# Optimization experiments

Measured on AMD Instinct MI355X. Metric: run time of the kernel, lower is better.

## Reference

```python
import jax, jax.numpy as jnp
import numpy as np

B, N, H, W = 4, 16, 480, 640
Hf, Wf, C = 120, 160, 128
NUM_CLASSES = 14
NUM_EXPERTS = NUM_CLASSES - 1  # 13 per-class ROI experts
ROI = 14  # ROI-align output resolution


def setup_inputs() -> dict:
    key = jax.random.key(0)
    ks = jax.random.split(key, 20)
    inp = {
        'depth': jax.random.normal(ks[0], (B, 1, H, W), jnp.float32),
        'context': jax.random.normal(ks[1], (B, 192, Hf, Wf), jnp.float32),
        'input_feature_map': jax.random.normal(ks[2], (B, C, Hf, Wf), jnp.float32),
        'bin_num': 64,
        'min_depth': 1,
        'max_depth': 10,
        'masks': jax.random.uniform(ks[3], (B, N, Hf, Wf), jnp.float32),
        'instances': jax.random.uniform(ks[4], (B, N, H, W), jnp.float32),
        'boxes': jax.random.uniform(ks[5], (B, N, 4), jnp.float32),
        'labels': jax.random.randint(ks[6], (B, N), 0, NUM_EXPERTS),
    }
    s = 0.05
    # per-class (expert) parameters, stacked on leading expert axis
    inp['w_conv_s'] = s * jax.random.normal(ks[7], (NUM_EXPERTS, C, C, 3, 3), jnp.float32)
    inp['b_conv_s'] = jnp.zeros((NUM_EXPERTS, C), jnp.float32)
    inp['w_fc'] = s * jax.random.normal(ks[8], (NUM_EXPERTS, 2, C), jnp.float32)
    inp['b_fc'] = jnp.zeros((NUM_EXPERTS, 2), jnp.float32)
    inp['w_conv_c1'] = s * jax.random.normal(ks[9], (NUM_EXPERTS, 64, C, 3, 3), jnp.float32)
    inp['b_conv_c1'] = jnp.zeros((NUM_EXPERTS, 64), jnp.float32)
    inp['w_conv_c2'] = s * jax.random.normal(ks[10], (NUM_EXPERTS, 1, 64, 3, 3), jnp.float32)
    inp['b_conv_c2'] = jnp.zeros((NUM_EXPERTS, 1), jnp.float32)
    return inp


def _boxes_norm(boxes_flat):
    # map raw rand [M,4] -> valid normalized (y1,x1,y2,x2) in [0,1]
    y1 = 0.6 * boxes_flat[:, 0]
    x1 = 0.6 * boxes_flat[:, 1]
    y2 = y1 + 0.1 + 0.3 * boxes_flat[:, 2]
    x2 = x1 + 0.1 + 0.3 * boxes_flat[:, 3]
    return y1, x1, y2, x2


def _roi_align(fmap, batch_idx, boxes_flat, R):
    # fmap [B,C,Hf,Wf] -> [M,C,R,R] bilinear ROI sampling (irregular gather)
    _, _, hf, wf = fmap.shape
    y1, x1, y2, x2 = _boxes_norm(boxes_flat)
    t = (jnp.arange(R, dtype=fmap.dtype) + 0.5) / R
    ys = (y1[:, None] + (y2 - y1)[:, None] * t) * (hf - 1)  # [M,R]
    xs = (x1[:, None] + (x2 - x1)[:, None] * t) * (wf - 1)
    y0 = jnp.clip(jnp.floor(ys).astype(jnp.int32), 0, hf - 2)
    x0 = jnp.clip(jnp.floor(xs).astype(jnp.int32), 0, wf - 2)
    wy = jnp.clip(ys - y0, 0.0, 1.0)[:, :, None, None]   # [M,R,1,1]
    wx = jnp.clip(xs - x0, 0.0, 1.0)[:, None, :, None]   # [M,1,R,1]
    b = batch_idx[:, None, None]
    Y0 = y0[:, :, None]
    X0 = x0[:, None, :]
    def g(dy, dx):
        return fmap[b, :, Y0 + dy, X0 + dx]  # [M,R,R,C]
    out = (g(0, 0) * (1 - wy) * (1 - wx) + g(0, 1) * (1 - wy) * wx
           + g(1, 0) * wy * (1 - wx) + g(1, 1) * wy * wx)
    return jnp.transpose(out, (0, 3, 1, 2))  # [M,C,R,R]


def _conv(x, w, b):
    # x [Cin,R,R], w [Cout,Cin,3,3] -> [Cout,R,R]
    y = jax.lax.conv_general_dilated(x[None], w, (1, 1), 'SAME',
                                     dimension_numbers=('NCHW', 'OIHW', 'NCHW'))[0]
    return y + b[:, None, None]

_conv_v = jax.vmap(_conv)  # per-instance expert conv (per-instance weights)


def reference(depth, context, input_feature_map, bin_num, min_depth, max_depth,
              masks, instances, boxes, labels,
              w_conv_s, b_conv_s, w_fc, b_fc, w_conv_c1, b_conv_c1, w_conv_c2, b_conv_c2):
    b_, n_, h, w = instances.shape
    M = b_ * n_
    lab = labels.reshape(M)
    batch_idx = jnp.repeat(jnp.arange(b_), n_)
    boxes_flat = boxes.reshape(M, 4)

    # shared ROI gather of class-routed instances
    roi = _roi_align(input_feature_map, batch_idx, boxes_flat, ROI)  # [M,C,R,R]

    # hard routing: gather each instance's class-expert weights by label
    hs = jax.nn.relu(_conv_v(roi, w_conv_s[lab], b_conv_s[lab]))     # [M,C,R,R]
    gap = hs.mean(axis=(2, 3))                                        # [M,C]
    ss = jnp.einsum('mc,moc->mo', gap, w_fc[lab]) + b_fc[lab]         # [M,2]
    scale = ss[:, 0].reshape(b_, n_)
    shift = ss[:, 1].reshape(b_, n_)

    h1 = jax.nn.relu(_conv_v(roi, w_conv_c1[lab], b_conv_c1[lab]))    # [M,64,R,R]
    c = _conv_v(h1, w_conv_c2[lab], b_conv_c2[lab])                   # [M,1,R,R]
    canonical = jax.image.resize(c, (M, 1, h, w), method='bilinear')
    canonical = canonical.reshape(b_, n_, h, w)

    # loss_type == 0: relu(.).clamp(min=0.001) == max(., 0.001)
    depth_r = jnp.maximum(canonical * scale[..., None, None] + shift[..., None, None], 0.001)
    return depth_r, canonical, scale, shift
```

## Files before the change

### kernel.cpp

```cpp
#include <hip/hip_runtime.h>


typedef unsigned short bfu;
typedef __attribute__((ext_vector_type(8))) short bf16x8;
typedef __attribute__((ext_vector_type(4))) float f32x4;

__device__ __forceinline__ float bf2f(bfu u) {
  union { unsigned int i; float f; } v;
  v.i = ((unsigned int)u) << 16;
  return v.f;
}
__device__ __forceinline__ bfu f2bf(float f) {
  union { float f; unsigned int i; } v;
  v.f = f;
  unsigned int u = v.i;
  u = (u + 0x7fffu + ((u >> 16) & 1u)) >> 16;
  return (bfu)u;
}

#define B_  4
#define N_  16
#define M_  64
#define H_  480
#define W_  640
#define HF  120
#define WF  160
#define C_  128
#define R_  14
#define PIX 196
#define NE  13
#define KK  1152

#define WS_XB    0
#define WS_XH    802816
#define WS_C     1204224
#define WS_GAP   1216768
#define WS_SCALE 1224960
#define WS_SHIFT 1225024
#define WS_WF    1225088
#define WS_BIASF 2662784
#define WS_W2    2665280
#define WS_B2    2672768
#define WS_WFC   2672784
#define WS_BFC   2676112

__global__ __launch_bounds__(256) void prep_kernel(
    const float* __restrict__ w_s, const float* __restrict__ b_s,
    const float* __restrict__ w_fc, const float* __restrict__ b_fc,
    const float* __restrict__ w_c1, const float* __restrict__ b_c1,
    const float* __restrict__ w_c2, const float* __restrict__ b_c2,
    float* __restrict__ ws)
{
  const int P0 = NE*192*KK;
  const int P1 = NE*192;
  const int P2 = NE*576;
  const int P3 = NE;
  const int P4 = NE*256;
  const int P5 = NE*2;
  const int P6 = M_*C_;
  int total = P0+P1+P2+P3+P4+P5+P6;
  bfu* wf = (bfu*)(ws + WS_WF);
  for (int idx = blockIdx.x*256 + threadIdx.x; idx < total; idx += gridDim.x*256) {
    int d = idx;
    if (d < P0) {
      int e = d / (192*KK);
      int r = d - e*(192*KK);
      int oc = r / KK;
      int k  = r - oc*KK;
      int kidx = k >> 7, ic = k & 127;
      float v = (oc < 128) ? w_s[((e*128 + oc)*128 + ic)*9 + kidx]
                           : w_c1[((e*64 + (oc-128))*128 + ic)*9 + kidx];
      wf[d] = f2bf(v);
      continue;
    }
    d -= P0;
    if (d < P1) {
      int e = d / 192, oc = d - e*192;
      ws[WS_BIASF + d] = (oc < 128) ? b_s[e*128 + oc] : b_c1[e*64 + oc - 128];
      continue;
    }
    d -= P1;
    if (d < P2) {
      int e = d / 576, k = d - e*576;
      int kidx = k >> 6, ic = k & 63;
      ws[WS_W2 + d] = w_c2[(e*64 + ic)*9 + kidx];
      continue;
    }
    d -= P2;
    if (d < P3) { ws[WS_B2 + d] = b_c2[d]; continue; }
    d -= P3;
    if (d < P4) { ws[WS_WFC + d] = w_fc[d]; continue; }
    d -= P4;
    if (d < P5) { ws[WS_BFC + d] = b_fc[d]; continue; }
    d -= P5;
    ws[WS_GAP + d] = 0.f;
  }
}

__global__ __launch_bounds__(256) void xb_kernel(
    const float* __restrict__ fmap, const float* __restrict__ boxes,
    float* __restrict__ ws)
{
  __shared__ int iy0[R_], ix0[R_];
  __shared__ float swy[R_], swx[R_];
  int m = blockIdx.x;
  int tid = threadIdx.x;
  if (tid < 2*R_) {
    int r = tid % R_;
    bool isY = tid < R_;
    float b0 = boxes[m*4 + (isY ? 0 : 1)];
    float b2 = boxes[m*4 + (isY ? 2 : 3)];
    float lo = 0.6f * b0;
    float hi = lo + 0.1f + 0.3f * b2;
    float t = ((float)r + 0.5f) / (float)R_;
    float dim = isY ? (float)(HF-1) : (float)(WF-1);
    float s = (lo + (hi - lo) * t) * dim;
    int maxi = isY ? (HF-2) : (WF-2);
    int i0 = (int)floorf(s);
    i0 = i0 < 0 ? 0 : (i0 > maxi ? maxi : i0);
    float w = s - (float)i0;
    w = w < 0.f ? 0.f : (w > 1.f ? 1.f : w);
    if (isY) { iy0[r] = i0; swy[r] = w; } else { ix0[r] = i0; swx[r] = w; }
  }
  __syncthreads();
  int bi = m / N_;
  const float* fb = fmap + (size_t)bi * C_ * HF * WF;
  bfu* xb = (bfu*)(ws + WS_XB);
  for (int idx = tid; idx < PIX*64; idx += 256) {
    int ic2 = (idx & 63) * 2;
    int p = idx >> 6;
    int ry = p / R_, rx = p - (p/R_)*R_;
    int y0 = iy0[ry], x0 = ix0[rx];
    float wy = swy[ry], wx = swx[rx];
    float w00 = (1.f-wy)*(1.f-wx), w01 = (1.f-wy)*wx;
    float w10 = wy*(1.f-wx),       w11 = wy*wx;
    bfu pk[2];
    #pragma unroll
    for (int u = 0; u < 2; ++u) {
      const float* f = fb + ((size_t)(ic2+u)*HF + y0)*WF + x0;
      float v = f[0]*w00 + f[1]*w01 + f[WF]*w10 + f[WF+1]*w11;
      pk[u] = f2bf(v);
    }
    *(ushort2*)&xb[((size_t)m*PIX + p)*128 + ic2] = make_ushort2(pk[0], pk[1]);
  }
}

__global__ __launch_bounds__(256) void gemm_kernel(
    const int* __restrict__ labels, float* __restrict__ ws)
{
  __shared__ bfu lA[128*32];
  __shared__ bfu lB[128*32];
  const bfu* Xb = (const bfu*)(ws + WS_XB);
  const bfu* WFp = (const bfu*)(ws + WS_WF);
  const float* biasf = ws + WS_BIASF;
  float* gap = ws + WS_GAP;
  bfu* Xh = (bfu*)(ws + WS_XH);

  int bx = blockIdx.x;
  int m  = bx >> 2;
  int mb = (bx >> 1) & 1;
  int nb = bx & 1;
  int e = labels[m];
  int tid = threadIdx.x;
  int wave = tid >> 6, lane = tid & 63;
  int wm = wave >> 1, wn = wave & 1;
  int l15 = lane & 15, q = lane >> 4;

  int row0 = tid >> 2, row1 = row0 + 64;
  int kc = tid & 3;
  int loff0 = row0*32 + (kc ^ ((row0 >> 1) & 3))*8;
  int loff1 = row1*32 + (kc ^ ((row1 >> 1) & 3))*8;
  int g0 = mb*128 + row0, g1 = mb*128 + row1;
  bool av0 = g0 < 192, av1 = g1 < 192;
  const bfu* wfe = WFp + (size_t)e*192*KK;
  const bfu* wr0 = wfe + (size_t)g0*KK + kc*8;
  const bfu* wr1 = wfe + (size_t)g1*KK + kc*8;
  int pg0 = nb*128 + row0, pg1 = nb*128 + row1;
  int py0 = pg0 / 14, px0 = pg0 - (pg0/14)*14;
  int py1 = pg1 / 14, px1 = pg1 - (pg1/14)*14;
  bool pv0 = pg0 < PIX, pv1 = pg1 < PIX;
  const bfu* xbm = Xb + (size_t)m*PIX*128;

  f32x4 acc[4][4];
  #pragma unroll
  for (int i = 0; i < 4; ++i)
    #pragma unroll
    for (int j = 0; j < 4; ++j)
      acc[i][j] = (f32x4){0.f, 0.f, 0.f, 0.f};

  const uint4 z4 = make_uint4(0,0,0,0);
  for (int s = 0; s < 36; ++s) {
    int kidx = s >> 2, icc = s & 3;
    int dy = kidx/3 - 1, dx = (kidx - (kidx/3)*3) - 1;
    uint4 a0 = av0 ? *(const uint4*)(wr0 + s*32) : z4;
    uint4 a1 = av1 ? *(const uint4*)(wr1 + s*32) : z4;
    int ys0 = py0 + dy, xs0 = px0 + dx;
    int ys1 = py1 + dy, xs1 = px1 + dx;
    bool v0 = pv0 && (unsigned)ys0 < 14u && (unsigned)xs0 < 14u;
    bool v1 = pv1 && (unsigned)ys1 < 14u && (unsigned)xs1 < 14u;
    uint4 b0 = v0 ? *(const uint4*)(xbm + (size_t)(ys0*14+xs0)*128 + icc*32 + kc*8) : z4;
    uint4 b1 = v1 ? *(const uint4*)(xbm + (size_t)(ys1*14+xs1)*128 + icc*32 + kc*8) : z4;
    __syncthreads();
    *(uint4*)&lA[loff0] = a0;
    *(uint4*)&lA[loff1] = a1;
    *(uint4*)&lB[loff0] = b0;
    *(uint4*)&lB[loff1] = b1;
    __syncthreads();
    bf16x8 af[4], bfr[4];
    #pragma unroll
    for (int i = 0; i < 4; ++i) {
      int r = wm*64 + i*16 + l15;
      af[i] = *(const bf16x8*)&lA[r*32 + (q ^ ((r >> 1) & 3))*8];
    }
    #pragma unroll
    for (int j = 0; j < 4; ++j) {
      int r = wn*64 + j*16 + l15;
      bfr[j] = *(const bf16x8*)&lB[r*32 + (q ^ ((r >> 1) & 3))*8];
    }
    #pragma unroll
    for (int i = 0; i < 4; ++i)
      #pragma unroll
      for (int j = 0; j < 4; ++j)
        acc[i][j] = __builtin_amdgcn_mfma_f32_16x16x32_bf16(af[i], bfr[j], acc[i][j], 0, 0, 0);
  }

  if (mb == 0) {
    #pragma unroll
    for (int i = 0; i < 4; ++i) {
      int ocb = wm*64 + i*16 + q*4;
      f32x4 bv = *(const f32x4*)&biasf[e*192 + ocb];
      #pragma unroll
      for (int r = 0; r < 4; ++r) {
        float sum = 0.f;
        #pragma unroll
        for (int j = 0; j < 4; ++j) {
          int p = nb*128 + wn*64 + j*16 + l15;
          float v = acc[i][j][r] + bv[r];
          v = v > 0.f ? v : 0.f;
          if (p < PIX) sum += v;
        }
        sum += __shfl_xor(sum, 1);
        sum += __shfl_xor(sum, 2);
        sum += __shfl_xor(sum, 4);
        sum += __shfl_xor(sum, 8);
        if (l15 == 0) atomicAdd(&gap[m*C_ + ocb + r], sum);
      }
    }
  } else if (wm == 0) {
    #pragma unroll
    for (int i = 0; i < 4; ++i) {
      int icb = i*16 + q*4;
      f32x4 bv = *(const f32x4*)&biasf[e*192 + 128 + icb];
      #pragma unroll
      for (int j = 0; j < 4; ++j) {
        int p = nb*128 + wn*64 + j*16 + l15;
        if (p < PIX) {
          ushort4 pk;
          float v0 = acc[i][j][0] + bv[0]; v0 = v0 > 0.f ? v0 : 0.f;
          float v1 = acc[i][j][1] + bv[1]; v1 = v1 > 0.f ? v1 : 0.f;
          float v2 = acc[i][j][2] + bv[2]; v2 = v2 > 0.f ? v2 : 0.f;
          float v3 = acc[i][j][3] + bv[3]; v3 = v3 > 0.f ? v3 : 0.f;
          pk.x = f2bf(v0); pk.y = f2bf(v1); pk.z = f2bf(v2); pk.w = f2bf(v3);
          *(ushort4*)&Xh[((size_t)m*PIX + p)*64 + icb] = pk;
        }
      }
    }
  }
}

__global__ __launch_bounds__(128) void fc_kernel(
    const int* __restrict__ labels, float* __restrict__ ws,
    float* __restrict__ out)
{
  int t = threadIdx.x;
  int m = t >> 1, o = t & 1;
  int e = labels[m];
  const float* g = ws + WS_GAP + m*C_;
  const float* wv = ws + WS_WFC + (e*2 + o)*C_;
  float s = 0.f;
  for (int c = 0; c < C_; ++c) s += g[c] * wv[c];
  s = ws[WS_BFC + e*2 + o] + s * (1.f/(float)PIX);
  size_t base = (size_t)2 * M_ * H_ * W_;
  if (o == 0) { ws[WS_SCALE + m] = s; out[base + m] = s; }
  else        { ws[WS_SHIFT + m] = s; out[base + M_ + m] = s; }
}

__global__ __launch_bounds__(256) void convc2_kernel(
    const int* __restrict__ labels, float* __restrict__ ws)
{
  __shared__ bfu xh[PIX*64];
  __shared__ float w2l[576];
  int m = blockIdx.x;
  int e = labels[m];
  int tid = threadIdx.x;
  const bfu* Xh = (const bfu*)(ws + WS_XH) + (size_t)m*PIX*64;
  for (int i = tid; i < PIX*64/8; i += 256)
    *(uint4*)&xh[i*8] = *(const uint4*)&Xh[i*8];
  for (int i = tid; i < 576; i += 256)
    w2l[i] = ws[WS_W2 + e*576 + i];
  __syncthreads();
  if (tid < PIX) {
    int y = tid / 14, x = tid - (tid/14)*14;
    float acc = 0.f;
    #pragma unroll
    for (int kidx = 0; kidx < 9; ++kidx) {
      int ys = y + kidx/3 - 1, xs = x + (kidx - (kidx/3)*3) - 1;
      if ((unsigned)ys < 14u && (unsigned)xs < 14u) {
        const bfu* xr = xh + (ys*14 + xs)*64;
        const float* wr = w2l + kidx*64;
        #pragma unroll
        for (int cc = 0; cc < 8; ++cc) {
          bf16x8 xv = *(const bf16x8*)&xr[cc*8];
          f32x4 wa = *(const f32x4*)&wr[cc*8];
          f32x4 wb = *(const f32x4*)&wr[cc*8 + 4];
          acc += bf2f((bfu)xv[0])*wa[0] + bf2f((bfu)xv[1])*wa[1]
               + bf2f((bfu)xv[2])*wa[2] + bf2f((bfu)xv[3])*wa[3]
               + bf2f((bfu)xv[4])*wb[0] + bf2f((bfu)xv[5])*wb[1]
               + bf2f((bfu)xv[6])*wb[2] + bf2f((bfu)xv[7])*wb[3];
        }
      }
    }
    ws[WS_C + m*PIX + tid] = acc + ws[WS_B2 + e];
  }
}

__global__ __launch_bounds__(256) void resize_kernel(
    const float* __restrict__ ws_c, const float* __restrict__ ws_scale,
    const float* __restrict__ ws_shift, float* __restrict__ out)
{
  __shared__ float cs[PIX];
  int bx = blockIdx.x;
  int m = bx / 150;
  int chunk = bx % 150;
  int tid = threadIdx.x;
  if (tid < PIX) cs[tid] = ws_c[m*PIX + tid];
  __syncthreads();
  float sc = ws_scale[m], sh = ws_shift[m];
  int q0 = chunk*2048 + tid*8;
  int y = q0 / W_;
  int x0i = q0 - y*W_;
  float py = ((float)y + 0.5f) * (14.f/(float)H_) - 0.5f;
  py = fminf(fmaxf(py, 0.f), 13.f);
  int y0 = (int)py; y0 = y0 > 12 ? 12 : y0;
  float wy = py - (float)y0;
  const float* r0 = cs + y0*R_;
  const float* r1 = r0 + R_;
  float vd[8], vc[8];
  #pragma unroll
  for (int u = 0; u < 8; ++u) {
    int x = x0i + u;
    float px = ((float)x + 0.5f) * (14.f/(float)W_) - 0.5f;
    px = fminf(fmaxf(px, 0.f), 13.f);
    int xq = (int)px; xq = xq > 12 ? 12 : xq;
    float wx = px - (float)xq;
    float v = (r0[xq]*(1.f-wx) + r0[xq+1]*wx) * (1.f-wy)
            + (r1[xq]*(1.f-wx) + r1[xq+1]*wx) * wy;
    vc[u] = v;
    vd[u] = fmaxf(v*sc + sh, 0.001f);
  }
  size_t base = (size_t)m * H_ * W_ + q0;
  float* od = out + base;
  float* oc = out + (size_t)M_*H_*W_ + base;
  *(float4*)(od)     = make_float4(vd[0], vd[1], vd[2], vd[3]);
  *(float4*)(od + 4) = make_float4(vd[4], vd[5], vd[6], vd[7]);
  *(float4*)(oc)     = make_float4(vc[0], vc[1], vc[2], vc[3]);
  *(float4*)(oc + 4) = make_float4(vc[4], vc[5], vc[6], vc[7]);
}

extern "C" void kernel_launch(void* const* d_in, const int* in_sizes, int n_in,
                              void* d_out, int out_size, void* d_ws, size_t ws_size,
                              hipStream_t stream) {
  const float* fmap  = (const float*)d_in[2];
  const float* boxes = (const float*)d_in[8];
  const int* labels  = (const int*)d_in[9];
  const float* w_s  = (const float*)d_in[10];
  const float* b_s  = (const float*)d_in[11];
  const float* w_fc = (const float*)d_in[12];
  const float* b_fc = (const float*)d_in[13];
  const float* w_c1 = (const float*)d_in[14];
  const float* b_c1 = (const float*)d_in[15];
  const float* w_c2 = (const float*)d_in[16];
  const float* b_c2 = (const float*)d_in[17];
  float* ws = (float*)d_ws;
  float* out = (float*)d_out;

  hipLaunchKernelGGL(prep_kernel, dim3(1024), dim3(256), 0, stream,
                     w_s, b_s, w_fc, b_fc, w_c1, b_c1, w_c2, b_c2, ws);
  hipLaunchKernelGGL(xb_kernel, dim3(M_), dim3(256), 0, stream,
                     fmap, boxes, ws);
  hipLaunchKernelGGL(gemm_kernel, dim3(M_*4), dim3(256), 0, stream,
                     labels, ws);
  hipLaunchKernelGGL(fc_kernel, dim3(1), dim3(128), 0, stream,
                     labels, ws, out);
  hipLaunchKernelGGL(convc2_kernel, dim3(M_), dim3(256), 0, stream,
                     labels, ws);
  hipLaunchKernelGGL(resize_kernel, dim3(M_*150), dim3(256), 0, stream,
                     ws + WS_C, ws + WS_SCALE, ws + WS_SHIFT, out);
}
```

Measured before the change: 393.6 us.

## Fuse prep with ROI gather, prefetch GEMM tiles, merge fc into convc2

Merges the weight-prep and ROI-align gather kernels into one launch. The gather now spreads across 256 blocks, each covering 32 channels of one ROI and staging its bf16 results through shared memory before writing them out. The GEMM loop register-prefetches the next K step's global loads so they overlap the MFMA work. The fc scale/shift reduction moves into the convc2 kernel as a wave shuffle reduction, and the resize output uses nontemporal stores. These changes cut launch count and hide global latency, at the cost of more registers in the GEMM and a more complex fused prep kernel.

```diff
diff --git a/kernel.cpp b/kernel.cpp
--- a/kernel.cpp
+++ b/kernel.cpp
@@ -44,13 +44,69 @@
 #define WS_WFC   2672784
 #define WS_BFC   2676112
 
-__global__ __launch_bounds__(256) void prep_kernel(
+#define XB_BLOCKS 256
+#define PREP_BLOCKS 1024
+
+__global__ __launch_bounds__(256) void prep_xb_kernel(
+    const float* __restrict__ fmap, const float* __restrict__ boxes,
     const float* __restrict__ w_s, const float* __restrict__ b_s,
     const float* __restrict__ w_fc, const float* __restrict__ b_fc,
     const float* __restrict__ w_c1, const float* __restrict__ b_c1,
     const float* __restrict__ w_c2, const float* __restrict__ b_c2,
     float* __restrict__ ws)
 {
+  int tid = threadIdx.x;
+  if (blockIdx.x < XB_BLOCKS) {
+    __shared__ int iy0[R_], ix0[R_];
+    __shared__ float swy[R_], swx[R_];
+    __shared__ unsigned int lt[PIX][17];
+    int m  = blockIdx.x >> 2;
+    int cb = (blockIdx.x & 3) * 32;
+    if (tid < 2*R_) {
+      int r = tid % R_;
+      bool isY = tid < R_;
+      float b0 = boxes[m*4 + (isY ? 0 : 1)];
+      float b2 = boxes[m*4 + (isY ? 2 : 3)];
+      float lo = 0.6f * b0;
+      float hi = lo + 0.1f + 0.3f * b2;
+      float t = ((float)r + 0.5f) / (float)R_;
+      float dim = isY ? (float)(HF-1) : (float)(WF-1);
+      float s = (lo + (hi - lo) * t) * dim;
+      int maxi = isY ? (HF-2) : (WF-2);
+      int i0 = (int)floorf(s);
+      i0 = i0 < 0 ? 0 : (i0 > maxi ? maxi : i0);
+      float w = s - (float)i0;
+      w = w < 0.f ? 0.f : (w > 1.f ? 1.f : w);
+      if (isY) { iy0[r] = i0; swy[r] = w; } else { ix0[r] = i0; swx[r] = w; }
+    }
+    __syncthreads();
+    int bi = m / N_;
+    const float* fb = fmap + ((size_t)bi * C_ + cb) * HF * WF;
+    if (tid < PIX) {
+      int ry = tid / 14, rx = tid - (tid/14)*14;
+      int y0 = iy0[ry], x0 = ix0[rx];
+      float wy = swy[ry], wx = swx[rx];
+      float w00 = (1.f-wy)*(1.f-wx), w01 = (1.f-wy)*wx;
+      float w10 = wy*(1.f-wx),       w11 = wy*wx;
+      const float* fp = fb + (size_t)y0*WF + x0;
+      #pragma unroll 4
+      for (int c2 = 0; c2 < 16; ++c2) {
+        const float* f0 = fp + (size_t)(2*c2)*HF*WF;
+        const float* f1 = f0 + (size_t)HF*WF;
+        float v0 = f0[0]*w00 + f0[1]*w01 + f0[WF]*w10 + f0[WF+1]*w11;
+        float v1 = f1[0]*w00 + f1[1]*w01 + f1[WF]*w10 + f1[WF+1]*w11;
+        lt[tid][c2] = (unsigned int)f2bf(v0) | ((unsigned int)f2bf(v1) << 16);
+      }
+    }
+    __syncthreads();
+    unsigned int* xbw = (unsigned int*)(ws + WS_XB);
+    for (int idx = tid; idx < PIX*16; idx += 256) {
+      int p = idx >> 4, c2 = idx & 15;
+      xbw[((size_t)m*PIX + p)*64 + (cb >> 1) + c2] = lt[p][c2];
+    }
+    return;
+  }
+
   const int P0 = NE*192*KK;
   const int P1 = NE*192;
   const int P2 = NE*576;
@@ -60,7 +116,8 @@
   const int P6 = M_*C_;
   int total = P0+P1+P2+P3+P4+P5+P6;
   bfu* wf = (bfu*)(ws + WS_WF);
-  for (int idx = blockIdx.x*256 + threadIdx.x; idx < total; idx += gridDim.x*256) {
+  for (int idx = (blockIdx.x - XB_BLOCKS)*256 + tid; idx < total;
+       idx += PREP_BLOCKS*256) {
     int d = idx;
     if (d < P0) {
       int e = d / (192*KK);
@@ -94,54 +151,6 @@
     if (d < P5) { ws[WS_BFC + d] = b_fc[d]; continue; }
     d -= P5;
     ws[WS_GAP + d] = 0.f;
-  }
-}
-
-__global__ __launch_bounds__(256) void xb_kernel(
-    const float* __restrict__ fmap, const float* __restrict__ boxes,
-    float* __restrict__ ws)
-{
-  __shared__ int iy0[R_], ix0[R_];
-  __shared__ float swy[R_], swx[R_];
-  int m = blockIdx.x;
-  int tid = threadIdx.x;
-  if (tid < 2*R_) {
-    int r = tid % R_;
-    bool isY = tid < R_;
-    float b0 = boxes[m*4 + (isY ? 0 : 1)];
-    float b2 = boxes[m*4 + (isY ? 2 : 3)];
-    float lo = 0.6f * b0;
-    float hi = lo + 0.1f + 0.3f * b2;
-    float t = ((float)r + 0.5f) / (float)R_;
-    float dim = isY ? (float)(HF-1) : (float)(WF-1);
-    float s = (lo + (hi - lo) * t) * dim;
-    int maxi = isY ? (HF-2) : (WF-2);
-    int i0 = (int)floorf(s);
-    i0 = i0 < 0 ? 0 : (i0 > maxi ? maxi : i0);
-    float w = s - (float)i0;
-    w = w < 0.f ? 0.f : (w > 1.f ? 1.f : w);
-    if (isY) { iy0[r] = i0; swy[r] = w; } else { ix0[r] = i0; swx[r] = w; }
-  }
-  __syncthreads();
-  int bi = m / N_;
-  const float* fb = fmap + (size_t)bi * C_ * HF * WF;
-  bfu* xb = (bfu*)(ws + WS_XB);
-  for (int idx = tid; idx < PIX*64; idx += 256) {
-    int ic2 = (idx & 63) * 2;
-    int p = idx >> 6;
-    int ry = p / R_, rx = p - (p/R_)*R_;
-    int y0 = iy0[ry], x0 = ix0[rx];
-    float wy = swy[ry], wx = swx[rx];
-    float w00 = (1.f-wy)*(1.f-wx), w01 = (1.f-wy)*wx;
-    float w10 = wy*(1.f-wx),       w11 = wy*wx;
-    bfu pk[2];
-    #pragma unroll
-    for (int u = 0; u < 2; ++u) {
-      const float* f = fb + ((size_t)(ic2+u)*HF + y0)*WF + x0;
-      float v = f[0]*w00 + f[1]*w01 + f[WF]*w10 + f[WF+1]*w11;
-      pk[u] = f2bf(v);
-    }
-    *(ushort2*)&xb[((size_t)m*PIX + p)*128 + ic2] = make_ushort2(pk[0], pk[1]);
   }
 }
 
@@ -189,23 +198,30 @@
       acc[i][j] = (f32x4){0.f, 0.f, 0.f, 0.f};
 
   const uint4 z4 = make_uint4(0,0,0,0);
-  for (int s = 0; s < 36; ++s) {
+  uint4 na0, na1, nb0, nb1;
+  auto issue = [&](int s, uint4& A0, uint4& A1, uint4& B0, uint4& B1) {
     int kidx = s >> 2, icc = s & 3;
-    int dy = kidx/3 - 1, dx = (kidx - (kidx/3)*3) - 1;
-    uint4 a0 = av0 ? *(const uint4*)(wr0 + s*32) : z4;
-    uint4 a1 = av1 ? *(const uint4*)(wr1 + s*32) : z4;
+    int t3 = kidx / 3;
+    int dy = t3 - 1, dx = (kidx - t3*3) - 1;
+    A0 = av0 ? *(const uint4*)(wr0 + s*32) : z4;
+    A1 = av1 ? *(const uint4*)(wr1 + s*32) : z4;
     int ys0 = py0 + dy, xs0 = px0 + dx;
     int ys1 = py1 + dy, xs1 = px1 + dx;
     bool v0 = pv0 && (unsigned)ys0 < 14u && (unsigned)xs0 < 14u;
     bool v1 = pv1 && (unsigned)ys1 < 14u && (unsigned)xs1 < 14u;
-    uint4 b0 = v0 ? *(const uint4*)(xbm + (size_t)(ys0*14+xs0)*128 + icc*32 + kc*8) : z4;
-    uint4 b1 = v1 ? *(const uint4*)(xbm + (size_t)(ys1*14+xs1)*128 + icc*32 + kc*8) : z4;
+    B0 = v0 ? *(const uint4*)(xbm + (size_t)(ys0*14+xs0)*128 + icc*32 + kc*8) : z4;
+    B1 = v1 ? *(const uint4*)(xbm + (size_t)(ys1*14+xs1)*128 + icc*32 + kc*8) : z4;
+  };
+  issue(0, na0, na1, nb0, nb1);
+
+  for (int s = 0; s < 36; ++s) {
     __syncthreads();
-    *(uint4*)&lA[loff0] = a0;
-    *(uint4*)&lA[loff1] = a1;
-    *(uint4*)&lB[loff0] = b0;
-    *(uint4*)&lB[loff1] = b1;
+    *(uint4*)&lA[loff0] = na0;
+    *(uint4*)&lA[loff1] = na1;
+    *(uint4*)&lB[loff0] = nb0;
+    *(uint4*)&lB[loff1] = nb1;
     __syncthreads();
+    if (s < 35) issue(s+1, na0, na1, nb0, nb1);
     bf16x8 af[4], bfr[4];
     #pragma unroll
     for (int i = 0; i < 4; ++i) {
@@ -268,31 +284,31 @@
   }
 }
 
-__global__ __launch_bounds__(128) void fc_kernel(
+__global__ __launch_bounds__(256) void convc2_kernel(
     const int* __restrict__ labels, float* __restrict__ ws,
     float* __restrict__ out)
-{
-  int t = threadIdx.x;
-  int m = t >> 1, o = t & 1;
-  int e = labels[m];
-  const float* g = ws + WS_GAP + m*C_;
-  const float* wv = ws + WS_WFC + (e*2 + o)*C_;
-  float s = 0.f;
-  for (int c = 0; c < C_; ++c) s += g[c] * wv[c];
-  s = ws[WS_BFC + e*2 + o] + s * (1.f/(float)PIX);
-  size_t base = (size_t)2 * M_ * H_ * W_;
-  if (o == 0) { ws[WS_SCALE + m] = s; out[base + m] = s; }
-  else        { ws[WS_SHIFT + m] = s; out[base + M_ + m] = s; }
-}
-
-__global__ __launch_bounds__(256) void convc2_kernel(
-    const int* __restrict__ labels, float* __restrict__ ws)
 {
   __shared__ bfu xh[PIX*64];
   __shared__ float w2l[576];
   int m = blockIdx.x;
   int e = labels[m];
   int tid = threadIdx.x;
+  int wave = tid >> 6, lane = tid & 63;
+
+  if (wave < 2) {
+    const float* g  = ws + WS_GAP + m*C_;
+    const float* wv = ws + WS_WFC + (e*2 + wave)*C_;
+    float s = g[lane]*wv[lane] + g[lane+64]*wv[lane+64];
+    #pragma unroll
+    for (int d = 32; d; d >>= 1) s += __shfl_xor(s, d);
+    if (lane == 0) {
+      s = ws[WS_BFC + e*2 + wave] + s * (1.f/(float)PIX);
+      size_t base = (size_t)2 * M_ * H_ * W_;
+      if (wave == 0) { ws[WS_SCALE + m] = s; out[base + m] = s; }
+      else           { ws[WS_SHIFT + m] = s; out[base + M_ + m] = s; }
+    }
+  }
+
   const bfu* Xh = (const bfu*)(ws + WS_XH) + (size_t)m*PIX*64;
   for (int i = tid; i < PIX*64/8; i += 256)
     *(uint4*)&xh[i*8] = *(const uint4*)&Xh[i*8];
@@ -361,10 +377,14 @@
   size_t base = (size_t)m * H_ * W_ + q0;
   float* od = out + base;
   float* oc = out + (size_t)M_*H_*W_ + base;
-  *(float4*)(od)     = make_float4(vd[0], vd[1], vd[2], vd[3]);
-  *(float4*)(od + 4) = make_float4(vd[4], vd[5], vd[6], vd[7]);
-  *(float4*)(oc)     = make_float4(vc[0], vc[1], vc[2], vc[3]);
-  *(float4*)(oc + 4) = make_float4(vc[4], vc[5], vc[6], vc[7]);
+  f32x4 d0 = (f32x4){vd[0], vd[1], vd[2], vd[3]};
+  f32x4 d1 = (f32x4){vd[4], vd[5], vd[6], vd[7]};
+  f32x4 c0 = (f32x4){vc[0], vc[1], vc[2], vc[3]};
+  f32x4 c1 = (f32x4){vc[4], vc[5], vc[6], vc[7]};
+  __builtin_nontemporal_store(d0, (f32x4*)(od));
+  __builtin_nontemporal_store(d1, (f32x4*)(od + 4));
+  __builtin_nontemporal_store(c0, (f32x4*)(oc));
+  __builtin_nontemporal_store(c1, (f32x4*)(oc + 4));
 }
 
 extern "C" void kernel_launch(void* const* d_in, const int* in_sizes, int n_in,
@@ -384,16 +404,12 @@
   float* ws = (float*)d_ws;
   float* out = (float*)d_out;
 
-  hipLaunchKernelGGL(prep_kernel, dim3(1024), dim3(256), 0, stream,
-                     w_s, b_s, w_fc, b_fc, w_c1, b_c1, w_c2, b_c2, ws);
-  hipLaunchKernelGGL(xb_kernel, dim3(M_), dim3(256), 0, stream,
-                     fmap, boxes, ws);
+  hipLaunchKernelGGL(prep_xb_kernel, dim3(XB_BLOCKS + PREP_BLOCKS), dim3(256), 0, stream,
+                     fmap, boxes, w_s, b_s, w_fc, b_fc, w_c1, b_c1, w_c2, b_c2, ws);
   hipLaunchKernelGGL(gemm_kernel, dim3(M_*4), dim3(256), 0, stream,
                      labels, ws);
-  hipLaunchKernelGGL(fc_kernel, dim3(1), dim3(128), 0, stream,
+  hipLaunchKernelGGL(convc2_kernel, dim3(M_), dim3(256), 0, stream,
                      labels, ws, out);
-  hipLaunchKernelGGL(convc2_kernel, dim3(M_), dim3(256), 0, stream,
-                     labels, ws);
   hipLaunchKernelGGL(resize_kernel, dim3(M_*150), dim3(256), 0, stream,
                      ws + WS_C, ws + WS_SCALE, ws + WS_SHIFT, out);
 }
```

After: 376.2 us (median of 2 runs). -4.4%, faster.
